# Performance work log

Hardware: AMD Instinct MI355X
Metric: run time of the kernel (lower is better)

Reference implementation:

```python
import jax, jax.numpy as jnp
import numpy as np

NUM_EMB = 1024
DIM = 256
BETA = 0.25


def setup_inputs() -> dict:
    key = jax.random.key(0)
    kx, kc = jax.random.split(key)
    x = jax.random.normal(kx, (32, DIM, 32, 32), dtype=jnp.float32)
    # nn.Parameter(...).uniform_(-1/num_emb, 1/num_emb)
    code_book = jax.random.uniform(kc, (NUM_EMB, DIM), dtype=jnp.float32,
                                   minval=-1.0 / NUM_EMB, maxval=1.0 / NUM_EMB)
    return {"x": x, "code_book": code_book}


def reference(x, code_book):
    b, c, h, w = x.shape
    # (b h w) c
    x_ = x.transpose(0, 2, 3, 1).reshape(-1, c)
    sq = jnp.sum(code_book ** 2, axis=-1)[None, :] + jnp.sum(x_ ** 2, axis=-1)[:, None]
    dist = sq - 2.0 * jnp.einsum('nc,kc->nk', x_, code_book)
    ids = jnp.argmin(dist, axis=-1).reshape(b, h, w)
    emb = code_book[ids]            # [b, h, w, c]
    emb = emb.transpose(0, 3, 1, 2)  # [b, c, h, w]
    dict_loss = jnp.mean((jax.lax.stop_gradient(x) - emb) ** 2)
    commitment_loss = BETA * jnp.mean((x - jax.lax.stop_gradient(emb)) ** 2)
    emb_loss = dict_loss + commitment_loss
    # straight-through estimator
    emb_st = x + jax.lax.stop_gradient(emb - x)
    return ids, emb_st, emb_loss
```

## Files before the change

### kernel.cpp

```cpp
#include <hip/hip_runtime.h>

#define NUM_EMB 1024
#define DIM     256
#define NPIX    32768
#define NELEM   8388608

typedef unsigned short u16;
typedef unsigned int   u32;
typedef __attribute__((ext_vector_type(8))) _Float16 f16x8;
typedef __attribute__((ext_vector_type(4))) float f32x4;

__device__ __forceinline__ u16 f32_f16(float f) {
    _Float16 h = (_Float16)f;
    return __builtin_bit_cast(u16, h);
}
__device__ __forceinline__ float f16_f32(u16 b) {
    return (float)__builtin_bit_cast(_Float16, b);
}


__global__ __launch_bounds__(256) void k_prep_x(const float* __restrict__ x,
        u16* __restrict__ Xa, u16* __restrict__ Xb,
        float* __restrict__ nx_out)
{
    __shared__ float nxp[4][64];
    const int t  = threadIdx.x;
    const int p  = t & 63;
    const int cq = t >> 6;
    const int bi = blockIdx.x;
    const int b  = bi >> 4;
    const int hw = ((bi & 15) << 6) + p;
    const float* xp = x + (((size_t)(b * 256 + cq * 64)) << 10) + hw;
    float s = 0.f;
    for (int i0 = 0; i0 < 64; i0 += 8) {
        u32 qa[4], qb[4];
#pragma unroll
        for (int j = 0; j < 8; ++j) {
            float v = xp[(size_t)(i0 + j) << 10];
            s = fmaf(v, v, s);
            float va = v * 0.25f;
            u16 ha = f32_f16(va);
            float rb = (va - f16_f32(ha)) * 1024.0f;
            u16 hb = f32_f16(rb);
            if ((j & 1) == 0) { qa[j>>1] = ha; qb[j>>1] = hb; }
            else { qa[j>>1] |= (u32)ha << 16; qb[j>>1] |= (u32)hb << 16; }
        }
        const int c = cq * 64 + i0;
        const size_t chunk = (((size_t)((c >> 5) * 4 + ((c >> 3) & 3))) << 15)
                             + (size_t)bi * 64 + p;
        *(uint4*)(Xa + chunk * 8) = make_uint4(qa[0], qa[1], qa[2], qa[3]);
        *(uint4*)(Xb + chunk * 8) = make_uint4(qb[0], qb[1], qb[2], qb[3]);
    }
    nxp[cq][p] = s;
    __syncthreads();
    if (t < 64)
        nx_out[bi * 64 + t] = ((nxp[0][t] + nxp[1][t]) + nxp[2][t]) + nxp[3][t];
}

__global__ __launch_bounds__(256) void k_prep_e(const float* __restrict__ cb,
        u16* __restrict__ Ea, u16* __restrict__ Ea2, u16* __restrict__ Eb2,
        float* __restrict__ ne_out)
{
    const int t = threadIdx.x;
    const int l32 = t & 31;
    const int code = blockIdx.x * 8 + (t >> 5);
    const float* cp = cb + (size_t)code * 256 + l32 * 8;
    u32 qa[4], qa2[4], qb2[4];
    float s = 0.f;
#pragma unroll
    for (int j = 0; j < 8; ++j) {
        float v = cp[j];
        s = fmaf(v, v, s);
        float va = v * 2048.0f;
        u16 ha = f32_f16(va);
        float rb = (va - f16_f32(ha)) * 1024.0f;
        u16 hb = f32_f16(rb);
        u16 ha2 = f32_f16(f16_f32(ha) * 9.765625e-04f);
        u16 hb2 = f32_f16(f16_f32(hb) * 9.765625e-04f);
        if ((j & 1) == 0) { qa[j>>1] = ha; qa2[j>>1] = ha2; qb2[j>>1] = hb2; }
        else { qa[j>>1] |= (u32)ha << 16; qa2[j>>1] |= (u32)ha2 << 16; qb2[j>>1] |= (u32)hb2 << 16; }
    }
    const size_t chunk = ((size_t)l32 << 10) + code;
    *(uint4*)(Ea  + chunk * 8) = make_uint4(qa[0],  qa[1],  qa[2],  qa[3]);
    *(uint4*)(Ea2 + chunk * 8) = make_uint4(qa2[0], qa2[1], qa2[2], qa2[3]);
    *(uint4*)(Eb2 + chunk * 8) = make_uint4(qb2[0], qb2[1], qb2[2], qb2[3]);
#pragma unroll
    for (int off = 16; off > 0; off >>= 1) s += __shfl_xor(s, off);
    if (l32 == 0) ne_out[code] = s;
}

__global__ __launch_bounds__(256, 5) void k_mfma_argmin(
        const u16* __restrict__ XA, const u16* __restrict__ XB,
        const u16* __restrict__ EA, const u16* __restrict__ EA2,
        const u16* __restrict__ EB2,
        const float* __restrict__ nx, const float* __restrict__ ne,
        float* __restrict__ partV, int* __restrict__ partI)
{
    __shared__ __align__(16) unsigned char ldsA[2][8192];
    __shared__ float redV[4][64];
    __shared__ int   redI[4][64];

    const int t = threadIdx.x;
    const int l = t & 63;
    const int w = t >> 6;

    const int bi   = blockIdx.x;
    const int xcd  = bi & 7;
    const int slot = bi >> 3;
    const int cT   = slot & 7;
    const int pT   = ((slot >> 3) << 3) | xcd;
    const int px0  = pT << 6;
    const int c0   = cT << 7;
    const int n0   = w << 5;
    const int kbl  = l >> 4;
    const int il   = l & 15;

    const u16* Xt[2] = {XA, XB};

    auto stageA = [&](int kc, int bf) {
#pragma unroll
        for (int q = 0; q < 2; ++q) {
            const int kb = t >> 6, px = t & 63;
            const u16* sa = Xt[q] + ((((size_t)(kc * 4 + kb)) << 15) + px0 + px) * 8;
            __builtin_amdgcn_global_load_lds(
                (const __attribute__((address_space(1))) void*)sa,
                (__attribute__((address_space(3))) void*)(&ldsA[bf][q * 4096 + t * 16]),
                16, 0, 0);
        }
    };

    f32x4 acc[4][2];
#pragma unroll
    for (int i = 0; i < 4; ++i)
#pragma unroll
        for (int j = 0; j < 2; ++j) acc[i][j] = (f32x4){0.f, 0.f, 0.f, 0.f};

    const size_t boff = (size_t)kbl * 8192 + (size_t)(c0 + n0 + il) * 8;
    const u16* pBa  = EA  + boff;
    const u16* pBa2 = EA2 + boff;
    const u16* pBb2 = EB2 + boff;

    stageA(0, 0);
    __syncthreads();

#pragma unroll
    for (int kc = 0; kc < 8; ++kc) {
        const int bf = kc & 1;
        if (kc < 7) stageA(kc + 1, bf ^ 1);

        f16x8 bqa[2], bq2a[2], bq2b[2];
#pragma unroll
        for (int ni = 0; ni < 2; ++ni) {
            const size_t o = (size_t)kc * 32768 + ni * 128;
            bqa[ni]  = *(const f16x8*)(pBa  + o);
            bq2a[ni] = *(const f16x8*)(pBa2 + o);
            bq2b[ni] = *(const f16x8*)(pBb2 + o);
        }

        __builtin_amdgcn_s_setprio(1);
#pragma unroll
        for (int mi = 0; mi < 4; ++mi) {
            const int fo = (kbl * 64 + mi * 16 + il) * 16;
            f16x8 afa = *(const f16x8*)(&ldsA[bf][fo]);
            f16x8 afb = *(const f16x8*)(&ldsA[bf][4096 + fo]);
#pragma unroll
            for (int ni = 0; ni < 2; ++ni) {
                acc[mi][ni] = __builtin_amdgcn_mfma_f32_16x16x32_f16(
                    afa, bqa[ni], acc[mi][ni], 0, 0, 0);
                acc[mi][ni] = __builtin_amdgcn_mfma_f32_16x16x32_f16(
                    afb, bq2a[ni], acc[mi][ni], 0, 0, 0);
                acc[mi][ni] = __builtin_amdgcn_mfma_f32_16x16x32_f16(
                    afa, bq2b[ni], acc[mi][ni], 0, 0, 0);
            }
        }
        __builtin_amdgcn_s_setprio(0);

        if (kc < 7) __syncthreads();
    }

    const int g = kbl, col = il;
    float nev[2];
#pragma unroll
    for (int ni = 0; ni < 2; ++ni) nev[ni] = ne[c0 + n0 + ni * 16 + col];
#pragma unroll
    for (int mi = 0; mi < 4; ++mi) {
#pragma unroll
        for (int r = 0; r < 4; ++r) {
            const int pxl = mi * 16 + g * 4 + r;
            const float nxv = nx[px0 + pxl];
            float best = 3.4e38f; int besti = 0;
#pragma unroll
            for (int ni = 0; ni < 2; ++ni) {
                float sc = (nxv + nev[ni]) - acc[mi][ni][r] * 3.90625e-03f;
                if (sc < best) { best = sc; besti = c0 + n0 + ni * 16 + col; }
            }
#pragma unroll
            for (int off = 1; off < 16; off <<= 1) {
                float ov = __shfl_xor(best, off);
                int   oi = __shfl_xor(besti, off);
                if (ov < best || (ov == best && oi < besti)) { best = ov; besti = oi; }
            }
            if (col == 0) { redV[w][pxl] = best; redI[w][pxl] = besti; }
        }
    }
    __syncthreads();
    if (t < 64) {
        float bv = redV[0][t]; int bidx = redI[0][t];
#pragma unroll
        for (int q = 1; q < 4; ++q) {
            float v = redV[q][t];
            int   i = redI[q][t];
            if (v < bv || (v == bv && i < bidx)) { bv = v; bidx = i; }
        }
        partV[cT * NPIX + px0 + t] = bv;
        partI[cT * NPIX + px0 + t] = bidx;
    }
}

__global__ __launch_bounds__(256) void k_outputs2(const float* __restrict__ x,
        const float* __restrict__ cb,
        const float* __restrict__ partV, const int* __restrict__ partI,
        float* __restrict__ ids_f, float* __restrict__ out_emb,
        float* __restrict__ partials)
{
    __shared__ int   ids_s[64];
    __shared__ float ev[64][65];
    __shared__ float sm[256];

    const int t  = threadIdx.x;
    const int w  = t >> 6, l = t & 63;
    const int bi = blockIdx.x;
    const int b  = bi >> 4;
    const int hw0 = (bi & 15) << 6;
    const int n0 = (b << 10) + hw0;

    if (t < 64) {
        const int px = n0 + t;
        float bv = partV[px]; int bix = partI[px];
#pragma unroll
        for (int ct = 1; ct < 8; ++ct) {
            float v = partV[ct * NPIX + px];
            int   i = partI[ct * NPIX + px];
            if (v < bv || (v == bv && i < bix)) { bv = v; bix = i; }
        }
        ids_f[px] = (float)bix;
        ids_s[t] = bix;
    }
    __syncthreads();

    float s = 0.f;
    for (int cc = 0; cc < 4; ++cc) {
#pragma unroll
        for (int pp = 0; pp < 16; ++pp) {
            const int px = w * 16 + pp;
            ev[px][l] = cb[(size_t)ids_s[px] * DIM + cc * 64 + l];
        }
        __syncthreads();
#pragma unroll
        for (int ci = 0; ci < 16; ++ci) {
            const int c  = cc * 64 + w * 16 + ci;
            const size_t xi = (((size_t)(b * DIM + c)) << 10) + hw0 + l;
            float xv = x[xi];
            float e  = ev[l][c & 63];
            out_emb[xi] = xv + (e - xv);
            float d = xv - e;
            s = fmaf(d, d, s);
        }
        __syncthreads();
    }
    sm[t] = s;
    __syncthreads();
    for (int off = 128; off > 0; off >>= 1) {
        if (t < off) sm[t] += sm[t + off];
        __syncthreads();
    }
    if (t == 0) partials[bi] = sm[0];
}

__global__ __launch_bounds__(256) void k_finalize(const float* __restrict__ partials,
                                                  int nparts,
                                                  float* __restrict__ out_loss)
{
    __shared__ float sm[256];
    const int tid = threadIdx.x;
    float s = 0.f;
    for (int k = tid; k < nparts; k += 256) s += partials[k];
    sm[tid] = s;
    __syncthreads();
    for (int off = 128; off > 0; off >>= 1) {
        if (tid < off) sm[tid] += sm[tid + off];
        __syncthreads();
    }
    if (tid == 0) {
        float m = sm[0] / (float)NELEM;
        out_loss[0] = m + 0.25f * m;
    }
}

__global__ __launch_bounds__(256) void k_enorm(const float* __restrict__ cb,
                                               float* __restrict__ enorm)
{
    const int tid  = threadIdx.x;
    const int lane = tid & 63;
    const int w    = tid >> 6;
    const int k    = blockIdx.x * 4 + w;
    const float* cp = cb + (size_t)k * DIM;
    float s = 0.f;
#pragma unroll
    for (int t = 0; t < 4; ++t) {
        float v = cp[lane + t * 64];
        s = fmaf(v, v, s);
    }
#pragma unroll
    for (int off = 32; off > 0; off >>= 1) s += __shfl_down(s, off);
    if (lane == 0) enorm[k] = s;
}

__global__ __launch_bounds__(256) void k_argmin(const float* __restrict__ x,
                                                const float* __restrict__ cb,
                                                const float* __restrict__ enorm,
                                                float* __restrict__ out_ids)
{
    __shared__ float xs[32][64];
    __shared__ float cbs[32][68];
    __shared__ float nx_l[64];
    __shared__ float nxp[4][64];
    __shared__ float red_v[64][17];
    __shared__ int   red_i[64][17];

    const int tid  = threadIdx.x;
    const int tx   = tid & 15;
    const int ty   = tid >> 4;
    const int pix0 = blockIdx.x * 64;
    const int b    = pix0 >> 10;
    const int hw0  = pix0 & 1023;

    {
        const int p = tid & 63, q = tid >> 6;
        float s = 0.f;
        const float* xp = x + ((size_t)(b * DIM + q * 64) * 1024) + hw0 + p;
        for (int c = 0; c < 64; ++c) {
            float v = xp[c * 1024];
            s = fmaf(v, v, s);
        }
        nxp[q][p] = s;
        __syncthreads();
        if (tid < 64)
            nx_l[tid] = ((nxp[0][tid] + nxp[1][tid]) + nxp[2][tid]) + nxp[3][tid];
        __syncthreads();
    }

    float nx_r[4];
#pragma unroll
    for (int i = 0; i < 4; ++i) nx_r[i] = nx_l[ty * 4 + i];

    float best_v[4];
    int   best_i[4];
#pragma unroll
    for (int i = 0; i < 4; ++i) { best_v[i] = 3.4e38f; best_i[i] = 0; }

    for (int cc = 0; cc < 16; ++cc) {
        float acc[4][4];
#pragma unroll
        for (int i = 0; i < 4; ++i)
#pragma unroll
            for (int j = 0; j < 4; ++j) acc[i][j] = 0.f;

        for (int kcc = 0; kcc < 8; ++kcc) {
            __syncthreads();
            {
                const int p = tid & 63, k0 = tid >> 6;
                const float* xp = x + ((size_t)(b * DIM + kcc * 32) * 1024) + hw0 + p;
#pragma unroll
                for (int tt = 0; tt < 8; ++tt) {
                    int kk = k0 + tt * 4;
                    xs[kk][p] = xp[kk * 1024];
                }
            }
            {
                const int kk = tid & 31, r0 = tid >> 5;
                const float* cp = cb + (size_t)(cc * 64) * DIM + kcc * 32 + kk;
#pragma unroll
                for (int tt = 0; tt < 8; ++tt) {
                    int r = r0 + tt * 8;
                    cbs[kk][r] = cp[r * DIM];
                }
            }
            __syncthreads();
#pragma unroll
            for (int kk = 0; kk < 32; ++kk) {
                float4 A = *(const float4*)&xs[kk][ty * 4];
                float4 B = *(const float4*)&cbs[kk][tx * 4];
                float a[4] = {A.x, A.y, A.z, A.w};
                float bb[4] = {B.x, B.y, B.z, B.w};
#pragma unroll
                for (int i = 0; i < 4; ++i)
#pragma unroll
                    for (int j = 0; j < 4; ++j)
                        acc[i][j] = fmaf(a[i], bb[j], acc[i][j]);
            }
        }

#pragma unroll
        for (int j = 0; j < 4; ++j) {
            const int code = cc * 64 + tx * 4 + j;
            const float nee = enorm[code];
#pragma unroll
            for (int i = 0; i < 4; ++i) {
                float s = (nx_r[i] + nee) - 2.0f * acc[i][j];
                if (s < best_v[i]) { best_v[i] = s; best_i[i] = code; }
            }
        }
    }

#pragma unroll
    for (int i = 0; i < 4; ++i) {
        red_v[ty * 4 + i][tx] = best_v[i];
        red_i[ty * 4 + i][tx] = best_i[i];
    }
    __syncthreads();
    if (tid < 64) {
        float bv = red_v[tid][0];
        int   bi = red_i[tid][0];
#pragma unroll
        for (int tt = 1; tt < 16; ++tt) {
            float v = red_v[tid][tt];
            int   idx = red_i[tid][tt];
            if (v < bv || (v == bv && idx < bi)) { bv = v; bi = idx; }
        }
        out_ids[pix0 + tid] = (float)bi;
    }
}

__global__ __launch_bounds__(256) void k_outputs(const float* __restrict__ x,
                                                 const float* __restrict__ cb,
                                                 const float* __restrict__ ids_f,
                                                 float* __restrict__ out_emb,
                                                 float* __restrict__ partials)
{
    const int tid = threadIdx.x;
    const int gid = blockIdx.x * 256 + tid;
    float s = 0.f;
#pragma unroll
    for (int it = 0; it < 4; ++it) {
        const int grp = gid + it * 524288;
        const int e0  = grp << 2;
        const int c   = (e0 >> 10) & 255;
        const int b   = e0 >> 18;
        const int hw  = e0 & 1023;
        const int n0  = (b << 10) + hw;
        float4 idv = *(const float4*)(ids_f + n0);
        float4 xv  = *(const float4*)(x + e0);
        float ev0 = cb[(int)idv.x * DIM + c];
        float ev1 = cb[(int)idv.y * DIM + c];
        float ev2 = cb[(int)idv.z * DIM + c];
        float ev3 = cb[(int)idv.w * DIM + c];
        float4 ov;
        ov.x = xv.x + (ev0 - xv.x);
        ov.y = xv.y + (ev1 - xv.y);
        ov.z = xv.z + (ev2 - xv.z);
        ov.w = xv.w + (ev3 - xv.w);
        *(float4*)(out_emb + e0) = ov;
        float d0 = xv.x - ev0, d1 = xv.y - ev1, d2 = xv.z - ev2, d3 = xv.w - ev3;
        s = fmaf(d0, d0, s); s = fmaf(d1, d1, s);
        s = fmaf(d2, d2, s); s = fmaf(d3, d3, s);
    }
    __shared__ float sm[256];
    sm[tid] = s;
    __syncthreads();
    for (int off = 128; off > 0; off >>= 1) {
        if (tid < off) sm[tid] += sm[tid + off];
        __syncthreads();
    }
    if (tid == 0) partials[blockIdx.x] = sm[0];
}

extern "C" void kernel_launch(void* const* d_in, const int* in_sizes, int n_in,
                              void* d_out, int out_size, void* d_ws, size_t ws_size,
                              hipStream_t stream)
{
    const float* x  = (const float*)d_in[0];
    const float* cb = (const float*)d_in[1];
    float* out   = (float*)d_out;
    float* ids_f = out;
    float* emb   = out + NPIX;
    float* loss  = out + NPIX + NELEM;

    char* wsb = (char*)d_ws;
    const size_t NEED = 37367808ull;
    if (ws_size >= NEED) {
        u16*   Xa  = (u16*)(wsb);
        u16*   Xb  = (u16*)(wsb + 16777216);
        u16*   Ea  = (u16*)(wsb + 33554432);
        u16*   Ea2 = (u16*)(wsb + 34078720);
        u16*   Eb2 = (u16*)(wsb + 34603008);
        float* nx  = (float*)(wsb + 35127296);
        float* ne  = (float*)(wsb + 35258368);
        float* pV  = (float*)(wsb + 35262464);
        int*   pI  = (int*)  (wsb + 36311040);
        float* lp  = (float*)(wsb + 37359616);
        k_prep_x    <<<512,  256, 0, stream>>>(x, Xa, Xb, nx);
        k_prep_e    <<<128,  256, 0, stream>>>(cb, Ea, Ea2, Eb2, ne);
        k_mfma_argmin<<<4096, 256, 0, stream>>>(Xa, Xb, Ea, Ea2, Eb2, nx, ne, pV, pI);
        k_outputs2  <<<512,  256, 0, stream>>>(x, cb, pV, pI, ids_f, emb, lp);
        k_finalize  <<<1,    256, 0, stream>>>(lp, 512, loss);
    } else {
        float* partials = (float*)wsb;
        float* enorm    = partials + 2048;
        k_enorm   <<<256,  256, 0, stream>>>(cb, enorm);
        k_argmin  <<<512,  256, 0, stream>>>(x, cb, enorm, ids_f);
        k_outputs <<<2048, 256, 0, stream>>>(x, cb, ids_f, emb, partials);
        k_finalize<<<1,    256, 0, stream>>>(partials, 2048, loss);
    }
}
```

Measured before the change: 107.3 us.

## Load X fragments directly from global instead of double-buffered LDS staging

Removes the LDS double buffer and global_load_lds staging of the X tiles, so each wave now loads its A fragments straight from global memory into registers. Per-iteration __syncthreads barriers go away with it. The occupancy hint drops from 5 to 4 blocks per SM to allow for the extra registers. In exchange, the four waves of a block each read the same X data from global/L2 separately, so reuse through LDS is lost and more memory traffic hits the cache hierarchy.

```diff
diff --git a/kernel.cpp b/kernel.cpp
--- a/kernel.cpp
+++ b/kernel.cpp
@@ -89,14 +89,13 @@
     if (l32 == 0) ne_out[code] = s;
 }
 
-__global__ __launch_bounds__(256, 5) void k_mfma_argmin(
+__global__ __launch_bounds__(256, 4) void k_mfma_argmin(
         const u16* __restrict__ XA, const u16* __restrict__ XB,
         const u16* __restrict__ EA, const u16* __restrict__ EA2,
         const u16* __restrict__ EB2,
         const float* __restrict__ nx, const float* __restrict__ ne,
         float* __restrict__ partV, int* __restrict__ partI)
 {
-    __shared__ __align__(16) unsigned char ldsA[2][8192];
     __shared__ float redV[4][64];
     __shared__ int   redI[4][64];
 
@@ -115,67 +114,52 @@
     const int kbl  = l >> 4;
     const int il   = l & 15;
 
-    const u16* Xt[2] = {XA, XB};
-
-    auto stageA = [&](int kc, int bf) {
-#pragma unroll
-        for (int q = 0; q < 2; ++q) {
-            const int kb = t >> 6, px = t & 63;
-            const u16* sa = Xt[q] + ((((size_t)(kc * 4 + kb)) << 15) + px0 + px) * 8;
-            __builtin_amdgcn_global_load_lds(
-                (const __attribute__((address_space(1))) void*)sa,
-                (__attribute__((address_space(3))) void*)(&ldsA[bf][q * 4096 + t * 16]),
-                16, 0, 0);
-        }
-    };
-
     f32x4 acc[4][2];
 #pragma unroll
     for (int i = 0; i < 4; ++i)
 #pragma unroll
         for (int j = 0; j < 2; ++j) acc[i][j] = (f32x4){0.f, 0.f, 0.f, 0.f};
 
-    const size_t boff = (size_t)kbl * 8192 + (size_t)(c0 + n0 + il) * 8;
+    const size_t aoff = (size_t)kbl * 262144 + (size_t)(px0 + il) * 8;
+    const size_t boff = (size_t)kbl * 8192   + (size_t)(c0 + n0 + il) * 8;
+    const u16* pXa  = XA  + aoff;
+    const u16* pXb  = XB  + aoff;
     const u16* pBa  = EA  + boff;
     const u16* pBa2 = EA2 + boff;
     const u16* pBb2 = EB2 + boff;
 
-    stageA(0, 0);
-    __syncthreads();
-
 #pragma unroll
     for (int kc = 0; kc < 8; ++kc) {
-        const int bf = kc & 1;
-        if (kc < 7) stageA(kc + 1, bf ^ 1);
-
+        const size_t ao = (size_t)kc * 1048576;
+        const size_t bo = (size_t)kc * 32768;
+
+        f16x8 afa[4], afb[4];
+#pragma unroll
+        for (int mi = 0; mi < 4; ++mi) {
+            afa[mi] = *(const f16x8*)(pXa + ao + mi * 128);
+            afb[mi] = *(const f16x8*)(pXb + ao + mi * 128);
+        }
         f16x8 bqa[2], bq2a[2], bq2b[2];
 #pragma unroll
         for (int ni = 0; ni < 2; ++ni) {
-            const size_t o = (size_t)kc * 32768 + ni * 128;
-            bqa[ni]  = *(const f16x8*)(pBa  + o);
-            bq2a[ni] = *(const f16x8*)(pBa2 + o);
-            bq2b[ni] = *(const f16x8*)(pBb2 + o);
+            bqa[ni]  = *(const f16x8*)(pBa  + bo + ni * 128);
+            bq2a[ni] = *(const f16x8*)(pBa2 + bo + ni * 128);
+            bq2b[ni] = *(const f16x8*)(pBb2 + bo + ni * 128);
         }
 
         __builtin_amdgcn_s_setprio(1);
 #pragma unroll
-        for (int mi = 0; mi < 4; ++mi) {
-            const int fo = (kbl * 64 + mi * 16 + il) * 16;
-            f16x8 afa = *(const f16x8*)(&ldsA[bf][fo]);
-            f16x8 afb = *(const f16x8*)(&ldsA[bf][4096 + fo]);
+        for (int mi = 0; mi < 4; ++mi)
 #pragma unroll
             for (int ni = 0; ni < 2; ++ni) {
                 acc[mi][ni] = __builtin_amdgcn_mfma_f32_16x16x32_f16(
-                    afa, bqa[ni], acc[mi][ni], 0, 0, 0);
+                    afa[mi], bqa[ni], acc[mi][ni], 0, 0, 0);
                 acc[mi][ni] = __builtin_amdgcn_mfma_f32_16x16x32_f16(
-                    afb, bq2a[ni], acc[mi][ni], 0, 0, 0);
+                    afb[mi], bq2a[ni], acc[mi][ni], 0, 0, 0);
                 acc[mi][ni] = __builtin_amdgcn_mfma_f32_16x16x32_f16(
-                    afa, bq2b[ni], acc[mi][ni], 0, 0, 0);
-            }
-        }
+                    afa[mi], bq2b[ni], acc[mi][ni], 0, 0, 0);
+            }
         __builtin_amdgcn_s_setprio(0);
-
-        if (kc < 7) __syncthreads();
     }
 
     const int g = kbl, col = il;
```

Result: slower. 112.2 us (+4.6%).

## Deepen LDS prefetch ring to four buffers and fuse prep kernels

Applied to the files above, without the earlier changes.

The mfma argmin kernel now stages A tiles into a 4-slot LDS ring with prefetch distance two. Full __syncthreads are replaced by explicit vmcnt waits plus raw s_barrier, which keeps one stage of loads in flight across the barrier. The separate x and codebook preparation kernels are merged into a single launch, split by block index. The doubled LDS footprint may lower resident blocks per CU.

```diff
diff --git a/kernel.cpp b/kernel.cpp
--- a/kernel.cpp
+++ b/kernel.cpp
@@ -19,74 +19,74 @@
 }
 
 
-__global__ __launch_bounds__(256) void k_prep_x(const float* __restrict__ x,
+__global__ __launch_bounds__(256) void k_prep(const float* __restrict__ x,
+        const float* __restrict__ cb,
         u16* __restrict__ Xa, u16* __restrict__ Xb,
-        float* __restrict__ nx_out)
+        u16* __restrict__ Ea, u16* __restrict__ Ea2, u16* __restrict__ Eb2,
+        float* __restrict__ nx_out, float* __restrict__ ne_out)
 {
     __shared__ float nxp[4][64];
     const int t  = threadIdx.x;
-    const int p  = t & 63;
-    const int cq = t >> 6;
     const int bi = blockIdx.x;
-    const int b  = bi >> 4;
-    const int hw = ((bi & 15) << 6) + p;
-    const float* xp = x + (((size_t)(b * 256 + cq * 64)) << 10) + hw;
-    float s = 0.f;
-    for (int i0 = 0; i0 < 64; i0 += 8) {
-        u32 qa[4], qb[4];
+
+    if (bi < 512) {
+        const int p  = t & 63;
+        const int cq = t >> 6;
+        const int b  = bi >> 4;
+        const int hw = ((bi & 15) << 6) + p;
+        const float* xp = x + (((size_t)(b * 256 + cq * 64)) << 10) + hw;
+        float s = 0.f;
+        for (int i0 = 0; i0 < 64; i0 += 8) {
+            u32 qa[4], qb[4];
+#pragma unroll
+            for (int j = 0; j < 8; ++j) {
+                float v = xp[(size_t)(i0 + j) << 10];
+                s = fmaf(v, v, s);
+                float va = v * 0.25f;
+                u16 ha = f32_f16(va);
+                float rb = (va - f16_f32(ha)) * 1024.0f;
+                u16 hb = f32_f16(rb);
+                if ((j & 1) == 0) { qa[j>>1] = ha; qb[j>>1] = hb; }
+                else { qa[j>>1] |= (u32)ha << 16; qb[j>>1] |= (u32)hb << 16; }
+            }
+            const int c = cq * 64 + i0;
+            const size_t chunk = (((size_t)((c >> 5) * 4 + ((c >> 3) & 3))) << 15)
+                                 + (size_t)bi * 64 + p;
+            *(uint4*)(Xa + chunk * 8) = make_uint4(qa[0], qa[1], qa[2], qa[3]);
+            *(uint4*)(Xb + chunk * 8) = make_uint4(qb[0], qb[1], qb[2], qb[3]);
+        }
+        nxp[cq][p] = s;
+        __syncthreads();
+        if (t < 64)
+            nx_out[bi * 64 + t] = ((nxp[0][t] + nxp[1][t]) + nxp[2][t]) + nxp[3][t];
+    } else {
+        const int bi2 = bi - 512;
+        const int l32 = t & 31;
+        const int code = bi2 * 8 + (t >> 5);
+        const float* cp = cb + (size_t)code * 256 + l32 * 8;
+        u32 qa[4], qa2[4], qb2[4];
+        float s = 0.f;
 #pragma unroll
         for (int j = 0; j < 8; ++j) {
-            float v = xp[(size_t)(i0 + j) << 10];
+            float v = cp[j];
             s = fmaf(v, v, s);
-            float va = v * 0.25f;
+            float va = v * 2048.0f;
             u16 ha = f32_f16(va);
             float rb = (va - f16_f32(ha)) * 1024.0f;
             u16 hb = f32_f16(rb);
-            if ((j & 1) == 0) { qa[j>>1] = ha; qb[j>>1] = hb; }
-            else { qa[j>>1] |= (u32)ha << 16; qb[j>>1] |= (u32)hb << 16; }
-        }
-        const int c = cq * 64 + i0;
-        const size_t chunk = (((size_t)((c >> 5) * 4 + ((c >> 3) & 3))) << 15)
-                             + (size_t)bi * 64 + p;
-        *(uint4*)(Xa + chunk * 8) = make_uint4(qa[0], qa[1], qa[2], qa[3]);
-        *(uint4*)(Xb + chunk * 8) = make_uint4(qb[0], qb[1], qb[2], qb[3]);
-    }
-    nxp[cq][p] = s;
-    __syncthreads();
-    if (t < 64)
-        nx_out[bi * 64 + t] = ((nxp[0][t] + nxp[1][t]) + nxp[2][t]) + nxp[3][t];
-}
-
-__global__ __launch_bounds__(256) void k_prep_e(const float* __restrict__ cb,
-        u16* __restrict__ Ea, u16* __restrict__ Ea2, u16* __restrict__ Eb2,
-        float* __restrict__ ne_out)
-{
-    const int t = threadIdx.x;
-    const int l32 = t & 31;
-    const int code = blockIdx.x * 8 + (t >> 5);
-    const float* cp = cb + (size_t)code * 256 + l32 * 8;
-    u32 qa[4], qa2[4], qb2[4];
-    float s = 0.f;
-#pragma unroll
-    for (int j = 0; j < 8; ++j) {
-        float v = cp[j];
-        s = fmaf(v, v, s);
-        float va = v * 2048.0f;
-        u16 ha = f32_f16(va);
-        float rb = (va - f16_f32(ha)) * 1024.0f;
-        u16 hb = f32_f16(rb);
-        u16 ha2 = f32_f16(f16_f32(ha) * 9.765625e-04f);
-        u16 hb2 = f32_f16(f16_f32(hb) * 9.765625e-04f);
-        if ((j & 1) == 0) { qa[j>>1] = ha; qa2[j>>1] = ha2; qb2[j>>1] = hb2; }
-        else { qa[j>>1] |= (u32)ha << 16; qa2[j>>1] |= (u32)ha2 << 16; qb2[j>>1] |= (u32)hb2 << 16; }
-    }
-    const size_t chunk = ((size_t)l32 << 10) + code;
-    *(uint4*)(Ea  + chunk * 8) = make_uint4(qa[0],  qa[1],  qa[2],  qa[3]);
-    *(uint4*)(Ea2 + chunk * 8) = make_uint4(qa2[0], qa2[1], qa2[2], qa2[3]);
-    *(uint4*)(Eb2 + chunk * 8) = make_uint4(qb2[0], qb2[1], qb2[2], qb2[3]);
-#pragma unroll
-    for (int off = 16; off > 0; off >>= 1) s += __shfl_xor(s, off);
-    if (l32 == 0) ne_out[code] = s;
+            u16 ha2 = f32_f16(f16_f32(ha) * 9.765625e-04f);
+            u16 hb2 = f32_f16(f16_f32(hb) * 9.765625e-04f);
+            if ((j & 1) == 0) { qa[j>>1] = ha; qa2[j>>1] = ha2; qb2[j>>1] = hb2; }
+            else { qa[j>>1] |= (u32)ha << 16; qa2[j>>1] |= (u32)ha2 << 16; qb2[j>>1] |= (u32)hb2 << 16; }
+        }
+        const size_t chunk = ((size_t)l32 << 10) + code;
+        *(uint4*)(Ea  + chunk * 8) = make_uint4(qa[0],  qa[1],  qa[2],  qa[3]);
+        *(uint4*)(Ea2 + chunk * 8) = make_uint4(qa2[0], qa2[1], qa2[2], qa2[3]);
+        *(uint4*)(Eb2 + chunk * 8) = make_uint4(qb2[0], qb2[1], qb2[2], qb2[3]);
+#pragma unroll
+        for (int off = 16; off > 0; off >>= 1) s += __shfl_xor(s, off);
+        if (l32 == 0) ne_out[code] = s;
+    }
 }
 
 __global__ __launch_bounds__(256, 5) void k_mfma_argmin(
@@ -96,7 +96,7 @@
         const float* __restrict__ nx, const float* __restrict__ ne,
         float* __restrict__ partV, int* __restrict__ partI)
 {
-    __shared__ __align__(16) unsigned char ldsA[2][8192];
+    __shared__ __align__(16) unsigned char ldsA[4][8192];
     __shared__ float redV[4][64];
     __shared__ int   redI[4][64];
 
@@ -141,12 +141,15 @@
     const u16* pBb2 = EB2 + boff;
 
     stageA(0, 0);
-    __syncthreads();
+    stageA(1, 1);
+    __builtin_amdgcn_sched_barrier(0);
+    asm volatile("s_waitcnt vmcnt(2)" ::: "memory");
+    __builtin_amdgcn_s_barrier();
+    __builtin_amdgcn_sched_barrier(0);
 
 #pragma unroll
     for (int kc = 0; kc < 8; ++kc) {
-        const int bf = kc & 1;
-        if (kc < 7) stageA(kc + 1, bf ^ 1);
+        const int bf = kc & 3;
 
         f16x8 bqa[2], bq2a[2], bq2b[2];
 #pragma unroll
@@ -156,6 +159,7 @@
             bq2a[ni] = *(const f16x8*)(pBa2 + o);
             bq2b[ni] = *(const f16x8*)(pBb2 + o);
         }
+        if (kc < 6) stageA(kc + 2, (kc + 2) & 3);
 
         __builtin_amdgcn_s_setprio(1);
 #pragma unroll
@@ -175,7 +179,15 @@
         }
         __builtin_amdgcn_s_setprio(0);
 
-        if (kc < 7) __syncthreads();
+        if (kc < 7) {
+            __builtin_amdgcn_sched_barrier(0);
+            if (kc < 6)
+                asm volatile("s_waitcnt vmcnt(2)" ::: "memory");
+            else
+                asm volatile("s_waitcnt vmcnt(0)" ::: "memory");
+            __builtin_amdgcn_s_barrier();
+            __builtin_amdgcn_sched_barrier(0);
+        }
     }
 
     const int g = kbl, col = il;
@@ -499,8 +511,7 @@
         float* pV  = (float*)(wsb + 35262464);
         int*   pI  = (int*)  (wsb + 36311040);
         float* lp  = (float*)(wsb + 37359616);
-        k_prep_x    <<<512,  256, 0, stream>>>(x, Xa, Xb, nx);
-        k_prep_e    <<<128,  256, 0, stream>>>(cb, Ea, Ea2, Eb2, ne);
+        k_prep      <<<640,  256, 0, stream>>>(x, cb, Xa, Xb, Ea, Ea2, Eb2, nx, ne);
         k_mfma_argmin<<<4096, 256, 0, stream>>>(Xa, Xb, Ea, Ea2, Eb2, nx, ne, pV, pI);
         k_outputs2  <<<512,  256, 0, stream>>>(x, cb, pV, pI, ids_f, emb, lp);
         k_finalize  <<<1,    256, 0, stream>>>(lp, 512, loss);
```

Measured after the change: 107.5 us. No clear change (+0.2%).
